# Kernel optimization log

Hardware: AMD Instinct MI355X
Metric: run time of the kernel (lower is better)

Reference implementation:

```python
import jax, jax.numpy as jnp
import numpy as np

N = 50000      # nodes
E = 400000     # edges
IN = 256       # in_dim
OUT = 64       # out_dim per head
ED = 64        # edge_dim
H = 4          # num_heads


def setup_inputs() -> dict:
    key = jax.random.key(0)
    ks = jax.random.split(key, 12)
    s = 0.05  # weight scale
    return {
        "x": jax.random.normal(ks[0], (N, IN), jnp.float32),
        "edge_index": jax.random.randint(ks[1], (2, E), 0, N),
        "edge_attr": jax.random.normal(ks[2], (E, ED), jnp.float32),
        # per-head stacked parameters
        "W_fc": jax.random.normal(ks[3], (H, IN, OUT), jnp.float32) * s,
        "b_fc": jnp.zeros((H, OUT), jnp.float32),
        "W_att": jax.random.normal(ks[4], (H, 2 * OUT + ED), jnp.float32) * s,
        "b_att": jnp.zeros((H,), jnp.float32),
        "W_edge": jax.random.normal(ks[5], (H, ED, OUT), jnp.float32) * s,
        "b_edge": jnp.zeros((H, OUT), jnp.float32),
        "W_eatt": jax.random.normal(ks[6], (H, ED, ED), jnp.float32) * s,
        "b_eatt": jnp.zeros((H, ED), jnp.float32),
    }


def reference(x, edge_index, edge_attr, W_fc, b_fc, W_att, b_att,
              W_edge, b_edge, W_eatt, b_eatt):
    src = edge_index[0]  # x_j (source / message sender)
    dst = edge_index[1]  # x_i (destination / aggregation index)

    # node transform per head: z[h] = x @ W_fc[h] + b_fc[h]   -> [H, N, OUT]
    z = jnp.einsum('ni,hio->hno', x, W_fc) + b_fc[:, None, :]
    # edge transform for attention calc: [H, E, ED]
    ea = jnp.einsum('ef,hfg->heg', edge_attr, W_eatt) + b_eatt[:, None, :]
    # edge transform for aggregation: [H, E, OUT]
    ez = jnp.einsum('ef,hfo->heo', edge_attr, W_edge) + b_edge[:, None, :]

    # attn_fc(cat[x_i, x_j, ea]) decomposed: W_att = [Wi | Wj | We]
    Wi = W_att[:, :OUT]            # [H, OUT]
    Wj = W_att[:, OUT:2 * OUT]     # [H, OUT]
    We = W_att[:, 2 * OUT:]        # [H, ED]
    a_node_i = jnp.einsum('hno,ho->hn', z, Wi)  # [H, N]
    a_node_j = jnp.einsum('hno,ho->hn', z, Wj)  # [H, N]
    a = (a_node_i[:, dst] + a_node_j[:, src]
         + jnp.einsum('heg,hg->he', ea, We) + b_att[:, None])  # [H, E]
    e = jax.nn.leaky_relu(a, negative_slope=0.2)

    # segment softmax over destination nodes, per head
    seg_max = jax.vmap(lambda v: jax.ops.segment_max(v, dst, num_segments=N))(e)
    exp_e = jnp.exp(e - seg_max[:, dst])
    seg_sum = jax.vmap(lambda v: jax.ops.segment_sum(v, dst, num_segments=N))(exp_e)
    alpha = exp_e / seg_sum[:, dst]  # [H, E]

    # weighted message: alpha * (x_j + ez), scatter-add to destination
    msg = alpha[:, :, None] * (z[:, src, :] + ez)  # [H, E, OUT]
    out = jax.vmap(lambda m: jax.ops.segment_sum(m, dst, num_segments=N))(msg)  # [H, N, OUT]

    # merge == 'cat' over heads -> [N, H*OUT]
    cat_out = jnp.transpose(out, (1, 0, 2)).reshape(N, H * OUT)
    return cat_out, alpha
```

## Files before the change

kernel.cpp:

```cpp
#include <hip/hip_runtime.h>
#include <math.h>

#define N_NODES 50000
#define N_EDGES 400000
#define IN_F 256
#define OUT_F 64
#define ED_F 64
#define NH 4
#define SCAN_NB ((N_NODES + 255) / 256)

using f16x8 = __attribute__((ext_vector_type(8))) _Float16;
using f32x4 = __attribute__((ext_vector_type(4))) float;

__global__ __launch_bounds__(256) void prep_kernel(
    const float* __restrict__ W_att, const float* __restrict__ b_att,
    const float* __restrict__ W_eatt, const float* __restrict__ b_eatt,
    const float* __restrict__ W_fc, const float* __restrict__ W_edge,
    float* __restrict__ u, float* __restrict__ c,
    _Float16* __restrict__ Wfcfrag, _Float16* __restrict__ Wefrag)
{
    const int b = blockIdx.x, t = threadIdx.x;
    if (b == 0) {
        int h = t >> 6, f = t & 63;
        const float* We = W_att + h * (2 * OUT_F + ED_F) + 2 * OUT_F;
        float s = 0.f;
        for (int g = 0; g < ED_F; g++) s += W_eatt[(h * ED_F + f) * ED_F + g] * We[g];
        u[t] = s;
        if (f == 0) {
            float cc = b_att[h];
            for (int g = 0; g < ED_F; g++) cc += b_eatt[h * ED_F + g] * We[g];
            c[h] = cc;
        }
    } else if (b <= 32) {
        int idx = b - 1;
        int h = idx >> 3, kt = idx & 7;
        int lane = t & 63, nt = t >> 6;
        int q = lane >> 4, l15 = lane & 15;
        f16x8 w;
#pragma unroll
        for (int j = 0; j < 8; j++) {
            int k = kt * 32 + q * 8 + j;
            int o = nt * 16 + l15;
            w[j] = (_Float16)W_fc[((size_t)h * IN_F + k) * OUT_F + o];
        }
        *(f16x8*)&Wfcfrag[(size_t)(((h * 8 + kt) * 4 + nt) * 64 + lane) * 8] = w;
    } else {
        int idx = b - 33;
        int h = idx >> 1, kt = idx & 1;
        int lane = t & 63, nt = t >> 6;
        int q = lane >> 4, l15 = lane & 15;
        f16x8 w;
#pragma unroll
        for (int j = 0; j < 8; j++) {
            int k = kt * 32 + q * 8 + j;
            int o = nt * 16 + l15;
            w[j] = (_Float16)W_edge[((size_t)h * ED_F + k) * OUT_F + o];
        }
        *(f16x8*)&Wefrag[(size_t)(((h * 2 + kt) * 4 + nt) * 64 + lane) * 8] = w;
    }
}

__global__ __launch_bounds__(256) void z_gemm(
    const float* __restrict__ x, const _Float16* __restrict__ Wfcfrag,
    const float* __restrict__ b_fc, const float* __restrict__ W_att,
    _Float16* __restrict__ zb, float* __restrict__ a_i, float* __restrict__ a_j)
{
    __shared__ _Float16 aLDS[32 * 64 * 8];
    const int t = threadIdx.x;
    const int n0 = blockIdx.x * 64;
    const int lane = t & 63, h = t >> 6;
    const int q = lane >> 4, l15 = lane & 15;

    {
        const int m = t >> 2, qq = t & 3;
        const int n = n0 + m;
#pragma unroll
        for (int p = 0; p < 4; p++) {
            float4 v4[4];
            if (n < N_NODES) {
                const float4* xp = (const float4*)(x + (size_t)n * IN_F + p * 64 + qq * 16);
#pragma unroll
                for (int k = 0; k < 4; k++) v4[k] = xp[k];
            } else {
#pragma unroll
                for (int k = 0; k < 4; k++) v4[k] = make_float4(0.f, 0.f, 0.f, 0.f);
            }
            const float* vv = (const float*)v4;
#pragma unroll
            for (int i = 0; i < 2; i++) {
                int c8 = p * 8 + qq * 2 + i;
                f16x8 w;
#pragma unroll
                for (int j = 0; j < 8; j++) w[j] = (_Float16)vv[i * 8 + j];
                *(f16x8*)&aLDS[(c8 * 64 + m) * 8] = w;
            }
        }
    }
    __syncthreads();

    f32x4 acc[4][4];
#pragma unroll
    for (int mt = 0; mt < 4; mt++)
#pragma unroll
        for (int nt = 0; nt < 4; nt++) acc[mt][nt] = (f32x4)0.f;

    for (int kt = 0; kt < 8; kt++) {
        f16x8 bfr[4];
#pragma unroll
        for (int nt = 0; nt < 4; nt++)
            bfr[nt] = *(const f16x8*)&Wfcfrag[(size_t)(((h * 8 + kt) * 4 + nt) * 64 + lane) * 8];
        f16x8 afr[4];
#pragma unroll
        for (int mt = 0; mt < 4; mt++)
            afr[mt] = *(f16x8*)&aLDS[((kt * 4 + q) * 64 + mt * 16 + l15) * 8];
#pragma unroll
        for (int mt = 0; mt < 4; mt++)
#pragma unroll
            for (int nt = 0; nt < 4; nt++)
                acc[mt][nt] = __builtin_amdgcn_mfma_f32_16x16x32_f16(afr[mt], bfr[nt], acc[mt][nt], 0, 0, 0);
    }

    float bfc[4], wiv[4], wjv[4];
#pragma unroll
    for (int nt = 0; nt < 4; nt++) {
        bfc[nt] = b_fc[h * OUT_F + nt * 16 + l15];
        wiv[nt] = W_att[h * 192 + nt * 16 + l15];
        wjv[nt] = W_att[h * 192 + 64 + nt * 16 + l15];
    }

#pragma unroll
    for (int mt = 0; mt < 4; mt++) {
#pragma unroll
        for (int r = 0; r < 4; r++) {
            const int node = n0 + mt * 16 + q * 4 + r;
            float zv[4];
            float pi = 0.f, pj = 0.f;
#pragma unroll
            for (int nt = 0; nt < 4; nt++) {
                zv[nt] = acc[mt][nt][r] + bfc[nt];
                pi += zv[nt] * wiv[nt];
                pj += zv[nt] * wjv[nt];
            }
#pragma unroll
            for (int m = 8; m; m >>= 1) {
                pi += __shfl_xor(pi, m, 64);
                pj += __shfl_xor(pj, m, 64);
            }
            if (node < N_NODES) {
                _Float16* zrow = zb + ((size_t)h * N_NODES + node) * OUT_F;
#pragma unroll
                for (int nt = 0; nt < 4; nt++)
                    zrow[nt * 16 + l15] = (_Float16)zv[nt];
                if (l15 == 0) {
                    a_i[h * N_NODES + node] = pi;
                    a_j[h * N_NODES + node] = pj;
                }
            }
        }
    }
}


__global__ __launch_bounds__(256) void hist_kernel(
    const int* __restrict__ edge_index, int* __restrict__ deg)
{
    const int e = blockIdx.x * 256 + threadIdx.x;
    if (e < N_EDGES) atomicAdd(&deg[edge_index[N_EDGES + e]], 1);
}

__global__ __launch_bounds__(256) void scan1_kernel(
    const int* __restrict__ deg, int* __restrict__ row_ptr, int* __restrict__ bsum)
{
    __shared__ int wsum[4];
    const int t = threadIdx.x, lane = t & 63, w = t >> 6;
    const int idx = blockIdx.x * 256 + t;
    int v = (idx < N_NODES) ? deg[idx] : 0;
    int x = v;
#pragma unroll
    for (int off = 1; off < 64; off <<= 1) {
        int y = __shfl_up(x, off, 64);
        if (lane >= off) x += y;
    }
    if (lane == 63) wsum[w] = x;
    __syncthreads();
    int woff = 0;
#pragma unroll
    for (int i = 0; i < 4; i++) if (i < w) woff += wsum[i];
    if (idx < N_NODES) row_ptr[idx] = woff + x - v;
    if (t == 255) bsum[blockIdx.x] = woff + x;
}

__global__ __launch_bounds__(256) void scan2_kernel(int* __restrict__ bsum)
{
    __shared__ int wsum[4];
    const int t = threadIdx.x, lane = t & 63, w = t >> 6;
    int v = (t < SCAN_NB) ? bsum[t] : 0;
    int x = v;
#pragma unroll
    for (int off = 1; off < 64; off <<= 1) {
        int y = __shfl_up(x, off, 64);
        if (lane >= off) x += y;
    }
    if (lane == 63) wsum[w] = x;
    __syncthreads();
    int woff = 0;
#pragma unroll
    for (int i = 0; i < 4; i++) if (i < w) woff += wsum[i];
    __syncthreads();
    if (t < SCAN_NB) bsum[t] = woff + x - v;
}

__global__ __launch_bounds__(256) void scan3_kernel(
    const int* __restrict__ bsum, int* __restrict__ row_ptr, int* __restrict__ cursor)
{
    const int idx = blockIdx.x * 256 + threadIdx.x;
    if (idx < N_NODES) {
        int rp = row_ptr[idx] + bsum[blockIdx.x];
        row_ptr[idx] = rp;
        cursor[idx] = rp;
    } else if (idx == N_NODES) {
        row_ptr[N_NODES] = N_EDGES;
    }
}

__global__ __launch_bounds__(256) void scatter_kernel(
    const int* __restrict__ edge_index, int* __restrict__ cursor,
    int* __restrict__ eorig, int* __restrict__ epos)
{
    const int e = blockIdx.x * 256 + threadIdx.x;
    if (e >= N_EDGES) return;
    const int d = edge_index[N_EDGES + e];
    const int pos = atomicAdd(&cursor[d], 1);
    eorig[pos] = e;
    epos[e] = pos;
}

__global__ __launch_bounds__(256) void fill_kernel(
    const int* __restrict__ edge_index, const int* __restrict__ eorig,
    int* __restrict__ ssrc, int* __restrict__ sdst)
{
    const int p = blockIdx.x * 256 + threadIdx.x;
    if (p >= N_EDGES) return;
    const int e = eorig[p];
    ssrc[p] = edge_index[e];
    sdst[p] = edge_index[N_EDGES + e];
}

__global__ __launch_bounds__(256) void logits_kernel(
    const int* __restrict__ ssrc, const int* __restrict__ sdst,
    const int* __restrict__ eorig, const float* __restrict__ edge_attr,
    const float* __restrict__ u, const float* __restrict__ c,
    const float* __restrict__ a_i, const float* __restrict__ a_j,
    float* __restrict__ eperm)
{
    __shared__ float uS[NH * ED_F];
    __shared__ float cS[NH];
    const int t = threadIdx.x;
    uS[t] = u[t];
    if (t < NH) cS[t] = c[t];
    __syncthreads();

    const int p = blockIdx.x * 256 + t;
    if (p >= N_EDGES) return;
    const int e = eorig[p];
    const int src = ssrc[p];
    const int dst = sdst[p];
    const float4* ap = (const float4*)(edge_attr + (size_t)e * ED_F);

    float acc[NH] = {0.f, 0.f, 0.f, 0.f};
#pragma unroll
    for (int j = 0; j < 16; j++) {
        const float4 v = ap[j];
#pragma unroll
        for (int h = 0; h < NH; h++) {
            const float4 uv = *(const float4*)&uS[h * ED_F + j * 4];
            acc[h] += v.x * uv.x + v.y * uv.y + v.z * uv.z + v.w * uv.w;
        }
    }
#pragma unroll
    for (int h = 0; h < NH; h++) {
        float a = acc[h] + a_i[h * N_NODES + dst] + a_j[h * N_NODES + src] + cS[h];
        float ev = a > 0.f ? a : 0.2f * a;
        eperm[(size_t)h * N_EDGES + p] = ev;
    }
}

__global__ __launch_bounds__(256) void stats_kernel(
    const int* __restrict__ row_ptr, const float* __restrict__ eperm,
    float* __restrict__ rmax, float* __restrict__ rinv)
{
    const int n = blockIdx.x * 256 + threadIdx.x;
    if (n >= N_NODES) return;
    const int b = row_ptr[n], en = row_ptr[n + 1];
    if (b >= en) return;
    const int h = blockIdx.y;
    const float* ep = eperm + (size_t)h * N_EDGES;
    float m = -INFINITY;
    for (int p = b; p < en; p++) m = fmaxf(m, ep[p]);
    float s = 0.f;
    for (int p = b; p < en; p++) s += __expf(ep[p] - m);
    rmax[h * N_NODES + n] = m;
    rinv[h * N_NODES + n] = 1.f / s;
}

__global__ __launch_bounds__(256) void alpha_orig_kernel(
    const int* __restrict__ edge_index, const int* __restrict__ epos,
    const float* __restrict__ eperm, const float* __restrict__ rmax,
    const float* __restrict__ rinv, float* __restrict__ ebuf)
{
    const int e = blockIdx.x * 256 + threadIdx.x;
    if (e >= N_EDGES) return;
    const int pos = epos[e];
    const int dst = edge_index[N_EDGES + e];
#pragma unroll
    for (int h = 0; h < NH; h++) {
        const float lg = eperm[(size_t)h * N_EDGES + pos];
        ebuf[(size_t)h * N_EDGES + e] =
            __expf(lg - rmax[h * N_NODES + dst]) * rinv[h * N_NODES + dst];
    }
}

__global__ __launch_bounds__(256) void aggregate_mfma(
    const int* __restrict__ ssrc, const int* __restrict__ sdst,
    const int* __restrict__ eorig, const float* __restrict__ edge_attr,
    const _Float16* __restrict__ Wefrag, const float* __restrict__ b_edge,
    const _Float16* __restrict__ zb, const float* __restrict__ eperm,
    const float* __restrict__ rmax, const float* __restrict__ rinv,
    float* __restrict__ out)
{
    __shared__ float tbuf[NH * 16 * 66];
    __shared__ int srcS[64], dstS[64];
    __shared__ float alphaS[NH][64];
    _Float16* aLDS = (_Float16*)tbuf;

    const int t = threadIdx.x;
    const int p0 = blockIdx.x * 64;
    const int lane = t & 63, h = t >> 6;
    const int q = lane >> 4, l15 = lane & 15;

    if (t < 64) srcS[t] = ssrc[p0 + t];
    else if (t < 128) dstS[t - 64] = sdst[p0 + t - 64];

    {
        const int m = t >> 2, qq = t & 3;
        const int er = eorig[p0 + m];
        const float4* ap = (const float4*)(edge_attr + (size_t)er * ED_F + qq * 16);
        float4 v4[4];
#pragma unroll
        for (int k = 0; k < 4; k++) v4[k] = ap[k];
        const float* vv = (const float*)v4;
#pragma unroll
        for (int i = 0; i < 2; i++) {
            int c8 = qq * 2 + i;
            f16x8 w;
#pragma unroll
            for (int j = 0; j < 8; j++) w[j] = (_Float16)vv[i * 8 + j];
            *(f16x8*)&aLDS[(c8 * 64 + m) * 8] = w;
        }
    }
    __syncthreads();

    {
        const int d = dstS[lane];
        const float lg = eperm[(size_t)h * N_EDGES + p0 + lane];
        alphaS[h][lane] = __expf(lg - rmax[h * N_NODES + d]) * rinv[h * N_NODES + d];
    }

    f16x8 wf[2][4];
#pragma unroll
    for (int kt = 0; kt < 2; kt++)
#pragma unroll
        for (int nt = 0; nt < 4; nt++)
            wf[kt][nt] = *(const f16x8*)&Wefrag[(size_t)(((h * 2 + kt) * 4 + nt) * 64 + lane) * 8];

    f32x4 acc[4][4];
#pragma unroll
    for (int mt = 0; mt < 4; mt++)
#pragma unroll
        for (int nt = 0; nt < 4; nt++) acc[mt][nt] = (f32x4)0.f;

#pragma unroll
    for (int kt = 0; kt < 2; kt++) {
        f16x8 afr[4];
#pragma unroll
        for (int mt = 0; mt < 4; mt++)
            afr[mt] = *(f16x8*)&aLDS[((kt * 4 + q) * 64 + mt * 16 + l15) * 8];
#pragma unroll
        for (int mt = 0; mt < 4; mt++)
#pragma unroll
            for (int nt = 0; nt < 4; nt++)
                acc[mt][nt] = __builtin_amdgcn_mfma_f32_16x16x32_f16(afr[mt], wf[kt][nt], acc[mt][nt], 0, 0, 0);
    }

    __syncthreads();

    const float beL = b_edge[h * OUT_F + lane];
    int cur = dstS[0];
    float accv = 0.f;

#pragma unroll
    for (int mt = 0; mt < 4; mt++) {
#pragma unroll
        for (int r = 0; r < 4; r++)
#pragma unroll
            for (int nt = 0; nt < 4; nt++)
                tbuf[(h * 16 + q * 4 + r) * 66 + nt * 16 + l15] = acc[mt][nt][r];

        float zf[16];
#pragma unroll
        for (int i = 0; i < 16; i++)
            zf[i] = (float)zb[((size_t)h * N_NODES + srcS[mt * 16 + i]) * OUT_F + lane];

#pragma unroll
        for (int i = 0; i < 16; i++) {
            const int el = mt * 16 + i;
            const int d = dstS[el];
            const float msg = tbuf[(h * 16 + i) * 66 + lane];
            if (d != cur) {
                atomicAdd(&out[(size_t)cur * (NH * OUT_F) + h * OUT_F + lane], accv);
                accv = 0.f;
                cur = d;
            }
            accv += alphaS[h][el] * (msg + beL + zf[i]);
        }
    }
    atomicAdd(&out[(size_t)cur * (NH * OUT_F) + h * OUT_F + lane], accv);
}

extern "C" void kernel_launch(void* const* d_in, const int* in_sizes, int n_in,
                              void* d_out, int out_size, void* d_ws, size_t ws_size,
                              hipStream_t stream) {
    const float* x         = (const float*)d_in[0];
    const int*   edge_index= (const int*)  d_in[1];
    const float* edge_attr = (const float*)d_in[2];
    const float* W_fc      = (const float*)d_in[3];
    const float* b_fc      = (const float*)d_in[4];
    const float* W_att     = (const float*)d_in[5];
    const float* b_att     = (const float*)d_in[6];
    const float* W_edge    = (const float*)d_in[7];
    const float* b_edge    = (const float*)d_in[8];
    const float* W_eatt    = (const float*)d_in[9];
    const float* b_eatt    = (const float*)d_in[10];

    float* out  = (float*)d_out;
    float* ebuf = out + (size_t)N_NODES * NH * OUT_F;

    _Float16* zb   = (_Float16*)d_ws;
    float* a_i     = (float*)(zb + (size_t)NH * N_NODES * OUT_F);
    float* a_j     = a_i + NH * N_NODES;
    float* rmax    = a_j + NH * N_NODES;
    float* rinv    = rmax + NH * N_NODES;
    float* eperm   = rinv + NH * N_NODES;
    float* u       = eperm + (size_t)NH * N_EDGES;
    float* c       = u + NH * 64;
    int* deg       = (int*)(c + NH);
    int* cursor    = deg + N_NODES;
    int* row_ptr   = cursor + N_NODES;
    int* epos      = row_ptr + (N_NODES + 16);
    int* eorig     = epos + N_EDGES;
    int* ssrc      = eorig + N_EDGES;
    int* sdst      = ssrc + N_EDGES;
    int* bsum      = sdst + N_EDGES;
    _Float16* Wfcfrag = (_Float16*)(bsum + 256);
    _Float16* Wefrag  = Wfcfrag + NH * 8 * 4 * 64 * 8;
    size_t need = (size_t)((char*)(Wefrag + NH * 2 * 4 * 64 * 8) - (char*)d_ws);

    hipMemsetAsync(out, 0, (size_t)N_NODES * NH * OUT_F * sizeof(float), stream);

    if (ws_size < need) {
        hipMemsetAsync(ebuf, 0, (size_t)NH * N_EDGES * sizeof(float), stream);
        return;
    }

    hipMemsetAsync(deg, 0, N_NODES * sizeof(int), stream);

    prep_kernel<<<41, 256, 0, stream>>>(W_att, b_att, W_eatt, b_eatt, W_fc, W_edge,
                                        u, c, Wfcfrag, Wefrag);

    hist_kernel<<<(N_EDGES + 255) / 256, 256, 0, stream>>>(edge_index, deg);
    scan1_kernel<<<SCAN_NB, 256, 0, stream>>>(deg, row_ptr, bsum);
    scan2_kernel<<<1, 256, 0, stream>>>(bsum);
    scan3_kernel<<<SCAN_NB, 256, 0, stream>>>(bsum, row_ptr, cursor);
    scatter_kernel<<<(N_EDGES + 255) / 256, 256, 0, stream>>>(edge_index, cursor,
                                                              eorig, epos);
    fill_kernel<<<(N_EDGES + 255) / 256, 256, 0, stream>>>(edge_index, eorig,
                                                           ssrc, sdst);

    z_gemm<<<(N_NODES + 63) / 64, 256, 0, stream>>>(x, Wfcfrag, b_fc, W_att,
                                                    zb, a_i, a_j);

    logits_kernel<<<(N_EDGES + 255) / 256, 256, 0, stream>>>(ssrc, sdst, eorig, edge_attr,
                                                             u, c, a_i, a_j, eperm);

    dim3 sg(SCAN_NB, NH);
    stats_kernel<<<sg, 256, 0, stream>>>(row_ptr, eperm, rmax, rinv);

    alpha_orig_kernel<<<(N_EDGES + 255) / 256, 256, 0, stream>>>(edge_index, epos,
                                                                 eperm, rmax, rinv, ebuf);

    aggregate_mfma<<<N_EDGES / 64, 256, 0, stream>>>(ssrc, sdst, eorig, edge_attr,
                                                     Wefrag, b_edge, zb, eperm,
                                                     rmax, rinv, out);
}
```

Baseline: 446.6 us.

## Fuse alpha output into aggregation, drop epos, load A fragments directly

Removes the separate alpha_orig kernel and the epos array: the aggregation kernel now writes alpha to the original edge order through eorig. The edge_attr A fragments are loaded straight into registers per lane instead of being staged through LDS, and the per-head src/dst/alpha values come from wave shuffles rather than shared arrays, which removes the barriers. The zb gathers are issued early around the MFMA loop, and interior destination segments are written with plain stores instead of atomics because they lie wholly inside a block. The trade-offs are much higher register pressure (64-entry zf, launch_bounds(256,1)) and scattered alpha writes.

```diff
diff --git a/kernel.cpp b/kernel.cpp
--- a/kernel.cpp
+++ b/kernel.cpp
@@ -225,14 +225,13 @@
 
 __global__ __launch_bounds__(256) void scatter_kernel(
     const int* __restrict__ edge_index, int* __restrict__ cursor,
-    int* __restrict__ eorig, int* __restrict__ epos)
+    int* __restrict__ eorig)
 {
     const int e = blockIdx.x * 256 + threadIdx.x;
     if (e >= N_EDGES) return;
     const int d = edge_index[N_EDGES + e];
     const int pos = atomicAdd(&cursor[d], 1);
     eorig[pos] = e;
-    epos[e] = pos;
 }
 
 __global__ __launch_bounds__(256) void fill_kernel(
@@ -303,67 +302,48 @@
     rinv[h * N_NODES + n] = 1.f / s;
 }
 
-__global__ __launch_bounds__(256) void alpha_orig_kernel(
-    const int* __restrict__ edge_index, const int* __restrict__ epos,
-    const float* __restrict__ eperm, const float* __restrict__ rmax,
-    const float* __restrict__ rinv, float* __restrict__ ebuf)
-{
-    const int e = blockIdx.x * 256 + threadIdx.x;
-    if (e >= N_EDGES) return;
-    const int pos = epos[e];
-    const int dst = edge_index[N_EDGES + e];
-#pragma unroll
-    for (int h = 0; h < NH; h++) {
-        const float lg = eperm[(size_t)h * N_EDGES + pos];
-        ebuf[(size_t)h * N_EDGES + e] =
-            __expf(lg - rmax[h * N_NODES + dst]) * rinv[h * N_NODES + dst];
-    }
-}
-
-__global__ __launch_bounds__(256) void aggregate_mfma(
+__global__ __launch_bounds__(256, 1) void aggregate_mfma(
     const int* __restrict__ ssrc, const int* __restrict__ sdst,
     const int* __restrict__ eorig, const float* __restrict__ edge_attr,
     const _Float16* __restrict__ Wefrag, const float* __restrict__ b_edge,
     const _Float16* __restrict__ zb, const float* __restrict__ eperm,
     const float* __restrict__ rmax, const float* __restrict__ rinv,
-    float* __restrict__ out)
-{
-    __shared__ float tbuf[NH * 16 * 66];
-    __shared__ int srcS[64], dstS[64];
-    __shared__ float alphaS[NH][64];
-    _Float16* aLDS = (_Float16*)tbuf;
+    float* __restrict__ ebuf, float* __restrict__ out)
+{
+    __shared__ float tbuf[NH][16 * 66];
 
     const int t = threadIdx.x;
     const int p0 = blockIdx.x * 64;
     const int lane = t & 63, h = t >> 6;
     const int q = lane >> 4, l15 = lane & 15;
 
-    if (t < 64) srcS[t] = ssrc[p0 + t];
-    else if (t < 128) dstS[t - 64] = sdst[p0 + t - 64];
-
-    {
-        const int m = t >> 2, qq = t & 3;
-        const int er = eorig[p0 + m];
-        const float4* ap = (const float4*)(edge_attr + (size_t)er * ED_F + qq * 16);
-        float4 v4[4];
-#pragma unroll
-        for (int k = 0; k < 4; k++) v4[k] = ap[k];
-        const float* vv = (const float*)v4;
-#pragma unroll
-        for (int i = 0; i < 2; i++) {
-            int c8 = qq * 2 + i;
+    const int mySrc = ssrc[p0 + lane];
+    const int myDst = sdst[p0 + lane];
+    const int myEor = eorig[p0 + lane];
+
+    const float lg = eperm[(size_t)h * N_EDGES + p0 + lane];
+    const float al = __expf(lg - rmax[h * N_NODES + myDst]) * rinv[h * N_NODES + myDst];
+    ebuf[(size_t)h * N_EDGES + myEor] = al;
+
+    int esh[4];
+#pragma unroll
+    for (int mt = 0; mt < 4; mt++) esh[mt] = __shfl(myEor, mt * 16 + l15);
+
+    f16x8 afr[2][4];
+#pragma unroll
+    for (int mt = 0; mt < 4; mt++) {
+        const float* rp = edge_attr + (size_t)esh[mt] * ED_F + q * 8;
+#pragma unroll
+        for (int kt = 0; kt < 2; kt++) {
+            const float4 v0 = *(const float4*)(rp + kt * 32);
+            const float4 v1 = *(const float4*)(rp + kt * 32 + 4);
             f16x8 w;
-#pragma unroll
-            for (int j = 0; j < 8; j++) w[j] = (_Float16)vv[i * 8 + j];
-            *(f16x8*)&aLDS[(c8 * 64 + m) * 8] = w;
-        }
-    }
-    __syncthreads();
-
-    {
-        const int d = dstS[lane];
-        const float lg = eperm[(size_t)h * N_EDGES + p0 + lane];
-        alphaS[h][lane] = __expf(lg - rmax[h * N_NODES + d]) * rinv[h * N_NODES + d];
+            w[0] = (_Float16)v0.x; w[1] = (_Float16)v0.y;
+            w[2] = (_Float16)v0.z; w[3] = (_Float16)v0.w;
+            w[4] = (_Float16)v1.x; w[5] = (_Float16)v1.y;
+            w[6] = (_Float16)v1.z; w[7] = (_Float16)v1.w;
+            afr[kt][mt] = w;
+        }
     }
 
     f16x8 wf[2][4];
@@ -373,6 +353,13 @@
         for (int nt = 0; nt < 4; nt++)
             wf[kt][nt] = *(const f16x8*)&Wefrag[(size_t)(((h * 2 + kt) * 4 + nt) * 64 + lane) * 8];
 
+    float zf[64];
+#pragma unroll
+    for (int i = 0; i < 32; i++) {
+        const int s = __shfl(mySrc, i);
+        zf[i] = (float)zb[((size_t)h * N_NODES + s) * OUT_F + lane];
+    }
+
     f32x4 acc[4][4];
 #pragma unroll
     for (int mt = 0; mt < 4; mt++)
@@ -380,23 +367,24 @@
         for (int nt = 0; nt < 4; nt++) acc[mt][nt] = (f32x4)0.f;
 
 #pragma unroll
-    for (int kt = 0; kt < 2; kt++) {
-        f16x8 afr[4];
+    for (int kt = 0; kt < 2; kt++)
 #pragma unroll
         for (int mt = 0; mt < 4; mt++)
-            afr[mt] = *(f16x8*)&aLDS[((kt * 4 + q) * 64 + mt * 16 + l15) * 8];
-#pragma unroll
-        for (int mt = 0; mt < 4; mt++)
 #pragma unroll
             for (int nt = 0; nt < 4; nt++)
-                acc[mt][nt] = __builtin_amdgcn_mfma_f32_16x16x32_f16(afr[mt], wf[kt][nt], acc[mt][nt], 0, 0, 0);
-    }
-
-    __syncthreads();
+                acc[mt][nt] = __builtin_amdgcn_mfma_f32_16x16x32_f16(afr[kt][mt], wf[kt][nt], acc[mt][nt], 0, 0, 0);
+
+#pragma unroll
+    for (int i = 32; i < 64; i++) {
+        const int s = __shfl(mySrc, i);
+        zf[i] = (float)zb[((size_t)h * N_NODES + s) * OUT_F + lane];
+    }
 
     const float beL = b_edge[h * OUT_F + lane];
-    int cur = dstS[0];
+    float* tb = tbuf[h];
+    int cur = __shfl(myDst, 0);
     float accv = 0.f;
+    bool first = true;
 
 #pragma unroll
     for (int mt = 0; mt < 4; mt++) {
@@ -404,24 +392,23 @@
         for (int r = 0; r < 4; r++)
 #pragma unroll
             for (int nt = 0; nt < 4; nt++)
-                tbuf[(h * 16 + q * 4 + r) * 66 + nt * 16 + l15] = acc[mt][nt][r];
-
-        float zf[16];
-#pragma unroll
-        for (int i = 0; i < 16; i++)
-            zf[i] = (float)zb[((size_t)h * N_NODES + srcS[mt * 16 + i]) * OUT_F + lane];
+                tb[(q * 4 + r) * 66 + nt * 16 + l15] = acc[mt][nt][r];
 
 #pragma unroll
         for (int i = 0; i < 16; i++) {
             const int el = mt * 16 + i;
-            const int d = dstS[el];
-            const float msg = tbuf[(h * 16 + i) * 66 + lane];
+            const int d = __shfl(myDst, el);
+            const float a = __shfl(al, el);
+            const float msg = tb[i * 66 + lane];
             if (d != cur) {
-                atomicAdd(&out[(size_t)cur * (NH * OUT_F) + h * OUT_F + lane], accv);
+                float* orow = &out[(size_t)cur * (NH * OUT_F) + h * OUT_F + lane];
+                if (first) atomicAdd(orow, accv);
+                else       *orow = accv;
+                first = false;
                 accv = 0.f;
                 cur = d;
             }
-            accv += alphaS[h][el] * (msg + beL + zf[i]);
+            accv += a * (msg + beL + zf[el]);
         }
     }
     atomicAdd(&out[(size_t)cur * (NH * OUT_F) + h * OUT_F + lane], accv);
@@ -456,8 +443,7 @@
     int* deg       = (int*)(c + NH);
     int* cursor    = deg + N_NODES;
     int* row_ptr   = cursor + N_NODES;
-    int* epos      = row_ptr + (N_NODES + 16);
-    int* eorig     = epos + N_EDGES;
+    int* eorig     = row_ptr + (N_NODES + 16);
     int* ssrc      = eorig + N_EDGES;
     int* sdst      = ssrc + N_EDGES;
     int* bsum      = sdst + N_EDGES;
@@ -481,8 +467,7 @@
     scan1_kernel<<<SCAN_NB, 256, 0, stream>>>(deg, row_ptr, bsum);
     scan2_kernel<<<1, 256, 0, stream>>>(bsum);
     scan3_kernel<<<SCAN_NB, 256, 0, stream>>>(bsum, row_ptr, cursor);
-    scatter_kernel<<<(N_EDGES + 255) / 256, 256, 0, stream>>>(edge_index, cursor,
-                                                              eorig, epos);
+    scatter_kernel<<<(N_EDGES + 255) / 256, 256, 0, stream>>>(edge_index, cursor, eorig);
     fill_kernel<<<(N_EDGES + 255) / 256, 256, 0, stream>>>(edge_index, eorig,
                                                            ssrc, sdst);
 
@@ -495,10 +480,7 @@
     dim3 sg(SCAN_NB, NH);
     stats_kernel<<<sg, 256, 0, stream>>>(row_ptr, eperm, rmax, rinv);
 
-    alpha_orig_kernel<<<(N_EDGES + 255) / 256, 256, 0, stream>>>(edge_index, epos,
-                                                                 eperm, rmax, rinv, ebuf);
-
     aggregate_mfma<<<N_EDGES / 64, 256, 0, stream>>>(ssrc, sdst, eorig, edge_attr,
                                                      Wefrag, b_edge, zb, eperm,
-                                                     rmax, rinv, out);
-}
+                                                     rmax, rinv, ebuf, out);
+}
```

Result: slower. 543.6 us (+21.7%).

## Store logits edge-major as float4 and normalize softmax in place

Applied to the files above, without the earlier changes.

Logits are now stored as one float4 per sorted edge (all heads together) instead of head-major arrays. A single softmax kernel computes max, sum and the normalized alpha in place, so the rmax/rinv arrays and the per-head stats grid go away. alpha_orig and aggregate then just read the precomputed alpha with one vector load instead of recomputing exp with gathered per-node stats. The deg memset is folded into prep_kernel. The softmax kernel now uses a quarter as many threads, each doing three passes, which may reduce parallelism for nodes with high degree.

```diff
diff --git a/kernel.cpp b/kernel.cpp
--- a/kernel.cpp
+++ b/kernel.cpp
@@ -17,7 +17,8 @@
     const float* __restrict__ W_eatt, const float* __restrict__ b_eatt,
     const float* __restrict__ W_fc, const float* __restrict__ W_edge,
     float* __restrict__ u, float* __restrict__ c,
-    _Float16* __restrict__ Wfcfrag, _Float16* __restrict__ Wefrag)
+    _Float16* __restrict__ Wfcfrag, _Float16* __restrict__ Wefrag,
+    int* __restrict__ deg)
 {
     const int b = blockIdx.x, t = threadIdx.x;
     if (b == 0) {
@@ -44,7 +45,7 @@
             w[j] = (_Float16)W_fc[((size_t)h * IN_F + k) * OUT_F + o];
         }
         *(f16x8*)&Wfcfrag[(size_t)(((h * 8 + kt) * 4 + nt) * 64 + lane) * 8] = w;
-    } else {
+    } else if (b <= 40) {
         int idx = b - 33;
         int h = idx >> 1, kt = idx & 1;
         int lane = t & 63, nt = t >> 6;
@@ -57,6 +58,9 @@
             w[j] = (_Float16)W_edge[((size_t)h * ED_F + k) * OUT_F + o];
         }
         *(f16x8*)&Wefrag[(size_t)(((h * 2 + kt) * 4 + nt) * 64 + lane) * 8] = w;
+    } else {
+        const int idx = (b - 41) * 256 + t;
+        if (idx < N_NODES) deg[idx] = 0;
     }
 }
 
@@ -251,7 +255,7 @@
     const int* __restrict__ eorig, const float* __restrict__ edge_attr,
     const float* __restrict__ u, const float* __restrict__ c,
     const float* __restrict__ a_i, const float* __restrict__ a_j,
-    float* __restrict__ eperm)
+    float4* __restrict__ epermT)
 {
     __shared__ float uS[NH * ED_F];
     __shared__ float cS[NH];
@@ -277,55 +281,62 @@
             acc[h] += v.x * uv.x + v.y * uv.y + v.z * uv.z + v.w * uv.w;
         }
     }
+    float4 ev;
+    float* evp = (float*)&ev;
 #pragma unroll
     for (int h = 0; h < NH; h++) {
         float a = acc[h] + a_i[h * N_NODES + dst] + a_j[h * N_NODES + src] + cS[h];
-        float ev = a > 0.f ? a : 0.2f * a;
-        eperm[(size_t)h * N_EDGES + p] = ev;
-    }
-}
-
-__global__ __launch_bounds__(256) void stats_kernel(
-    const int* __restrict__ row_ptr, const float* __restrict__ eperm,
-    float* __restrict__ rmax, float* __restrict__ rinv)
+        evp[h] = a > 0.f ? a : 0.2f * a;
+    }
+    epermT[p] = ev;
+}
+
+__global__ __launch_bounds__(256) void softmax_kernel(
+    const int* __restrict__ row_ptr, float4* __restrict__ epermT)
 {
     const int n = blockIdx.x * 256 + threadIdx.x;
     if (n >= N_NODES) return;
     const int b = row_ptr[n], en = row_ptr[n + 1];
     if (b >= en) return;
-    const int h = blockIdx.y;
-    const float* ep = eperm + (size_t)h * N_EDGES;
-    float m = -INFINITY;
-    for (int p = b; p < en; p++) m = fmaxf(m, ep[p]);
-    float s = 0.f;
-    for (int p = b; p < en; p++) s += __expf(ep[p] - m);
-    rmax[h * N_NODES + n] = m;
-    rinv[h * N_NODES + n] = 1.f / s;
+
+    float4 m4 = make_float4(-INFINITY, -INFINITY, -INFINITY, -INFINITY);
+    for (int p = b; p < en; p++) {
+        const float4 v = epermT[p];
+        m4.x = fmaxf(m4.x, v.x); m4.y = fmaxf(m4.y, v.y);
+        m4.z = fmaxf(m4.z, v.z); m4.w = fmaxf(m4.w, v.w);
+    }
+    float4 s4 = make_float4(0.f, 0.f, 0.f, 0.f);
+    for (int p = b; p < en; p++) {
+        const float4 v = epermT[p];
+        s4.x += __expf(v.x - m4.x); s4.y += __expf(v.y - m4.y);
+        s4.z += __expf(v.z - m4.z); s4.w += __expf(v.w - m4.w);
+    }
+    const float4 i4 = make_float4(1.f / s4.x, 1.f / s4.y, 1.f / s4.z, 1.f / s4.w);
+    for (int p = b; p < en; p++) {
+        const float4 v = epermT[p];
+        epermT[p] = make_float4(__expf(v.x - m4.x) * i4.x, __expf(v.y - m4.y) * i4.y,
+                                __expf(v.z - m4.z) * i4.z, __expf(v.w - m4.w) * i4.w);
+    }
 }
 
 __global__ __launch_bounds__(256) void alpha_orig_kernel(
-    const int* __restrict__ edge_index, const int* __restrict__ epos,
-    const float* __restrict__ eperm, const float* __restrict__ rmax,
-    const float* __restrict__ rinv, float* __restrict__ ebuf)
+    const int* __restrict__ epos, const float4* __restrict__ epermT,
+    float* __restrict__ ebuf)
 {
     const int e = blockIdx.x * 256 + threadIdx.x;
     if (e >= N_EDGES) return;
-    const int pos = epos[e];
-    const int dst = edge_index[N_EDGES + e];
-#pragma unroll
-    for (int h = 0; h < NH; h++) {
-        const float lg = eperm[(size_t)h * N_EDGES + pos];
-        ebuf[(size_t)h * N_EDGES + e] =
-            __expf(lg - rmax[h * N_NODES + dst]) * rinv[h * N_NODES + dst];
-    }
+    const float4 a = epermT[epos[e]];
+    ebuf[e] = a.x;
+    ebuf[(size_t)N_EDGES + e] = a.y;
+    ebuf[(size_t)2 * N_EDGES + e] = a.z;
+    ebuf[(size_t)3 * N_EDGES + e] = a.w;
 }
 
 __global__ __launch_bounds__(256) void aggregate_mfma(
     const int* __restrict__ ssrc, const int* __restrict__ sdst,
     const int* __restrict__ eorig, const float* __restrict__ edge_attr,
     const _Float16* __restrict__ Wefrag, const float* __restrict__ b_edge,
-    const _Float16* __restrict__ zb, const float* __restrict__ eperm,
-    const float* __restrict__ rmax, const float* __restrict__ rinv,
+    const _Float16* __restrict__ zb, const float4* __restrict__ epermT,
     float* __restrict__ out)
 {
     __shared__ float tbuf[NH * 16 * 66];
@@ -340,6 +351,11 @@
 
     if (t < 64) srcS[t] = ssrc[p0 + t];
     else if (t < 128) dstS[t - 64] = sdst[p0 + t - 64];
+
+    {
+        const float4 a4 = epermT[p0 + lane];
+        alphaS[h][lane] = ((const float*)&a4)[h];
+    }
 
     {
         const int m = t >> 2, qq = t & 3;
@@ -360,12 +376,6 @@
     }
     __syncthreads();
 
-    {
-        const int d = dstS[lane];
-        const float lg = eperm[(size_t)h * N_EDGES + p0 + lane];
-        alphaS[h][lane] = __expf(lg - rmax[h * N_NODES + d]) * rinv[h * N_NODES + d];
-    }
-
     f16x8 wf[2][4];
 #pragma unroll
     for (int kt = 0; kt < 2; kt++)
@@ -395,6 +405,7 @@
     __syncthreads();
 
     const float beL = b_edge[h * OUT_F + lane];
+    float* tb = &tbuf[h * 16 * 66];
     int cur = dstS[0];
     float accv = 0.f;
 
@@ -404,7 +415,7 @@
         for (int r = 0; r < 4; r++)
 #pragma unroll
             for (int nt = 0; nt < 4; nt++)
-                tbuf[(h * 16 + q * 4 + r) * 66 + nt * 16 + l15] = acc[mt][nt][r];
+                tb[(q * 4 + r) * 66 + nt * 16 + l15] = acc[mt][nt][r];
 
         float zf[16];
 #pragma unroll
@@ -415,7 +426,7 @@
         for (int i = 0; i < 16; i++) {
             const int el = mt * 16 + i;
             const int d = dstS[el];
-            const float msg = tbuf[(h * 16 + i) * 66 + lane];
+            const float msg = tb[i * 66 + lane];
             if (d != cur) {
                 atomicAdd(&out[(size_t)cur * (NH * OUT_F) + h * OUT_F + lane], accv);
                 accv = 0.f;
@@ -446,12 +457,10 @@
     float* ebuf = out + (size_t)N_NODES * NH * OUT_F;
 
     _Float16* zb   = (_Float16*)d_ws;
-    float* a_i     = (float*)(zb + (size_t)NH * N_NODES * OUT_F);
+    float4* epermT = (float4*)(zb + (size_t)NH * N_NODES * OUT_F);
+    float* a_i     = (float*)(epermT + N_EDGES);
     float* a_j     = a_i + NH * N_NODES;
-    float* rmax    = a_j + NH * N_NODES;
-    float* rinv    = rmax + NH * N_NODES;
-    float* eperm   = rinv + NH * N_NODES;
-    float* u       = eperm + (size_t)NH * N_EDGES;
+    float* u       = a_j + NH * N_NODES;
     float* c       = u + NH * 64;
     int* deg       = (int*)(c + NH);
     int* cursor    = deg + N_NODES;
@@ -472,10 +481,9 @@
         return;
     }
 
-    hipMemsetAsync(deg, 0, N_NODES * sizeof(int), stream);
-
-    prep_kernel<<<41, 256, 0, stream>>>(W_att, b_att, W_eatt, b_eatt, W_fc, W_edge,
-                                        u, c, Wfcfrag, Wefrag);
+    prep_kernel<<<41 + SCAN_NB, 256, 0, stream>>>(W_att, b_att, W_eatt, b_eatt,
+                                                  W_fc, W_edge, u, c,
+                                                  Wfcfrag, Wefrag, deg);
 
     hist_kernel<<<(N_EDGES + 255) / 256, 256, 0, stream>>>(edge_index, deg);
     scan1_kernel<<<SCAN_NB, 256, 0, stream>>>(deg, row_ptr, bsum);
@@ -490,15 +498,12 @@
                                                     zb, a_i, a_j);
 
     logits_kernel<<<(N_EDGES + 255) / 256, 256, 0, stream>>>(ssrc, sdst, eorig, edge_attr,
-                                                             u, c, a_i, a_j, eperm);
-
-    dim3 sg(SCAN_NB, NH);
-    stats_kernel<<<sg, 256, 0, stream>>>(row_ptr, eperm, rmax, rinv);
-
-    alpha_orig_kernel<<<(N_EDGES + 255) / 256, 256, 0, stream>>>(edge_index, epos,
-                                                                 eperm, rmax, rinv, ebuf);
+                                                             u, c, a_i, a_j, epermT);
+
+    softmax_kernel<<<SCAN_NB, 256, 0, stream>>>(row_ptr, epermT);
+
+    alpha_orig_kernel<<<(N_EDGES + 255) / 256, 256, 0, stream>>>(epos, epermT, ebuf);
 
     aggregate_mfma<<<N_EDGES / 64, 256, 0, stream>>>(ssrc, sdst, eorig, edge_attr,
-                                                     Wefrag, b_edge, zb, eperm,
-                                                     rmax, rinv, out);
-}
+                                                     Wefrag, b_edge, zb, epermT, out);
+}
```

Result: faster. 430.1 us (-3.7%).
